# Performance work log

Measured on AMD Instinct MI355X. Metric: run time of the kernel, lower is better.

The kernel has to match this reference:

```python
import jax, jax.numpy as jnp
import numpy as np

HEADS = 16
DIM_HEAD = 64
SCALE = DIM_HEAD ** -0.5


def setup_inputs() -> dict:
    key = jax.random.key(0)
    k1, k2, k3, k4 = jax.random.split(key, 4)
    b, n, dim = 2, 2048, 1024
    inner = HEADS * DIM_HEAD  # 1024
    x = jax.random.normal(k1, (b, n, dim), dtype=jnp.float32)
    mask = jax.random.randint(k2, (b, n), 0, 2, dtype=jnp.int32)
    Wqkv = jax.random.normal(k3, (dim, inner), dtype=jnp.float32) * (dim ** -0.5)
    Wout = jax.random.normal(k4, (inner, dim), dtype=jnp.float32) * (inner ** -0.5)
    bout = jnp.zeros((dim,), dtype=jnp.float32)
    return {"x": x, "mask": mask, "Wqkv": Wqkv, "Wout": Wout, "bout": bout}


def reference(x, mask, Wqkv, Wout, bout):
    b, n, _ = x.shape
    # shared projection: w acts as q = k = v (CRATE subspace attention)
    w = jnp.einsum('bnd,de->bne', x, Wqkv)
    w = w.reshape(b, n, HEADS, DIM_HEAD).transpose(0, 2, 1, 3)  # b h n d
    dots = jnp.einsum('bhid,bhjd->bhij', w, w) * SCALE           # b h n n
    attn = jax.nn.softmax(dots, axis=-1)
    # post-softmax multiplicative masking (mask=1 zeros the column)
    m = mask[:, None, None, :].astype(attn.dtype)
    attn = attn * (1.0 - m)
    out = jnp.einsum('bhij,bhjd->bhid', attn, w)                 # b h n d
    out = out.transpose(0, 2, 1, 3).reshape(b, n, HEADS * DIM_HEAD)
    return jnp.einsum('bne,ed->bnd', out, Wout) + bout
```

## Files before the change

kernel.cpp:

```cpp
#include <hip/hip_runtime.h>
#include <hip/hip_bf16.h>
#include <stdint.h>

typedef unsigned short u16;
typedef unsigned int u32;
typedef __bf16 bf16x8 __attribute__((ext_vector_type(8)));
typedef float f32x4 __attribute__((ext_vector_type(4)));
typedef float f32x16 __attribute__((ext_vector_type(16)));
typedef u32 u32x4 __attribute__((ext_vector_type(4)));

#define AS1 __attribute__((address_space(1)))
#define AS3 __attribute__((address_space(3)))

__device__ __forceinline__ void async16(const u16* g, u16* l) {
  __builtin_amdgcn_global_load_lds((const AS1 uint32_t*)(const void*)g,
                                   (AS3 uint32_t*)l, 16, 0, 0);
}

__device__ __forceinline__ u16 f2bf(float v) {
  union { __hip_bfloat16 b; u16 u; } c; c.b = __float2bfloat16(v); return c.u;
}

__device__ __forceinline__ u32 pkbf(float a, float b) {
  u32 r;
  asm("v_cvt_pk_bf16_f32 %0, %1, %2" : "=v"(r) : "v"(a), "v"(b));
  return r;
}

__device__ __forceinline__ void swap32(u32 &a, u32 &b) {
  asm("v_permlane32_swap_b32 %0, %1" : "+v"(a), "+v"(b));
}

#if __has_builtin(__builtin_amdgcn_exp2f)
#define fast_exp2(x) __builtin_amdgcn_exp2f(x)
#else
#define fast_exp2(x) exp2f(x)
#endif

#if __has_builtin(__builtin_amdgcn_rcpf)
#define fast_rcp(x) __builtin_amdgcn_rcpf(x)
#else
#define fast_rcp(x) (1.0f / (x))
#endif

__device__ __forceinline__ uint4 pack8(float4 lo, float4 hi) {
  uint4 q;
  q.x = (u32)f2bf(lo.x) | ((u32)f2bf(lo.y) << 16);
  q.y = (u32)f2bf(lo.z) | ((u32)f2bf(lo.w) << 16);
  q.z = (u32)f2bf(hi.x) | ((u32)f2bf(hi.y) << 16);
  q.w = (u32)f2bf(hi.z) | ((u32)f2bf(hi.w) << 16);
  return q;
}

__global__ void cvt_x(const float* __restrict__ in, u16* __restrict__ out) {
  int i = (blockIdx.x * 256 + threadIdx.x) * 8;
  float4 lo = *(const float4*)(in + i);
  float4 hi = *(const float4*)(in + i + 4);
  *(uint4*)(out + i) = pack8(lo, hi);
}

__global__ void transpose1024_cvt2(const float* __restrict__ in0, u16* __restrict__ out0,
                                   const float* __restrict__ in1, u16* __restrict__ out1) {
  const float* in = blockIdx.z ? in1 : in0;
  u16* out = blockIdx.z ? out1 : out0;
  __shared__ u16 tile[32][33];
  int tx = threadIdx.x, ty = threadIdx.y;
  int c0 = blockIdx.x * 32, r0 = blockIdx.y * 32;
#pragma unroll
  for (int i = 0; i < 32; i += 8)
    tile[ty + i][tx] = f2bf(in[(size_t)(r0 + ty + i) * 1024 + c0 + tx]);
  __syncthreads();
#pragma unroll
  for (int i = 0; i < 32; i += 8)
    out[(size_t)(c0 + ty + i) * 1024 + r0 + tx] = tile[tx][ty + i];
}

__global__ void scale_transpose_v(const u16* __restrict__ w, const int* __restrict__ mask,
                                  u16* __restrict__ Vt) {
  __shared__ u16 tile[32][33];
  const int tx = threadIdx.x, ty = threadIdx.y;
  const int j0 = blockIdx.x * 32, d0 = blockIdx.y * 32;
  const int bh = blockIdx.z, b = bh >> 4, hc = (bh & 15) * 64;
#pragma unroll
  for (int i = 0; i < 32; i += 8) {
    int j = j0 + ty + i;
    u16 v = w[(size_t)(b * 2048 + j) * 1024 + hc + d0 + tx];
    tile[ty + i][tx] = mask[b * 2048 + j] ? (u16)0 : v;
  }
  __syncthreads();
#pragma unroll
  for (int i = 0; i < 32; i += 8)
    Vt[((size_t)bh * 64 + d0 + ty + i) * 2048 + j0 + tx] = tile[tx][ty + i];
}

template<bool OUT_F32>
__launch_bounds__(256)
__global__ void gemm_bt(const u16* __restrict__ A, const u16* __restrict__ BT,
                        void* __restrict__ Cp, const float* __restrict__ bias,
                        int M, int N, int K) {
  __shared__ __align__(16) u16 As[2][128 * 32];
  __shared__ __align__(16) u16 Bs[2][64 * 32];
  const int t = threadIdx.x;
  const int lane = t & 63, wave = t >> 6;
  const int m0 = blockIdx.x * 128, n0 = blockIdx.y * 64;
  const int wm = (wave & 1) * 64, wn = (wave >> 1) * 32;
  const int lrow = lane & 15, quad = lane >> 4;

  f32x4 acc[4][2] = {};

  const int ar = t >> 2, ac = (t & 3) * 8;
  const u16* gA = A + (size_t)(m0 + ar) * K + ac;
  const u16* gB = BT + (size_t)(n0 + ar) * K + ac;

  for (int k0 = 0; k0 < K; k0 += 64) {
    async16(gA + k0,                       &As[0][t * 8]);
    async16(gA + k0 + (size_t)64 * K,      &As[0][t * 8 + 2048]);
    async16(gA + k0 + 32,                  &As[1][t * 8]);
    async16(gA + k0 + 32 + (size_t)64 * K, &As[1][t * 8 + 2048]);
    async16(gB + k0,                       &Bs[0][t * 8]);
    async16(gB + k0 + 32,                  &Bs[1][t * 8]);
    __syncthreads();

#pragma unroll
    for (int kk = 0; kk < 2; kk++) {
      bf16x8 af[4], bfr[2];
#pragma unroll
      for (int i = 0; i < 4; i++)
        af[i] = *(const bf16x8*)&As[kk][(wm + i * 16 + lrow) * 32 + quad * 8];
#pragma unroll
      for (int j = 0; j < 2; j++)
        bfr[j] = *(const bf16x8*)&Bs[kk][(wn + j * 16 + lrow) * 32 + quad * 8];
#pragma unroll
      for (int i = 0; i < 4; i++)
#pragma unroll
        for (int j = 0; j < 2; j++)
          acc[i][j] = __builtin_amdgcn_mfma_f32_16x16x32_bf16(af[i], bfr[j], acc[i][j], 0, 0, 0);
    }
    __syncthreads();
  }

  float bv[2];
#pragma unroll
  for (int j = 0; j < 2; j++)
    bv[j] = bias ? bias[n0 + wn + j * 16 + lrow] : 0.f;

#pragma unroll
  for (int i = 0; i < 4; i++) {
#pragma unroll
    for (int r = 0; r < 4; r++) {
      int row = m0 + wm + i * 16 + quad * 4 + r;
#pragma unroll
      for (int j = 0; j < 2; j++) {
        size_t ci = (size_t)row * N + n0 + wn + j * 16 + lrow;
        float v = acc[i][j][r] + bv[j];
        if (OUT_F32) ((float*)Cp)[ci] = v;
        else ((u16*)Cp)[ci] = f2bf(v);
      }
    }
  }
}

#define C1 0.18033688f
#define C2 -28.853901f
__launch_bounds__(512)
__global__ void attn_kernel(const u16* __restrict__ w, const u16* __restrict__ Vt,
                            u16* __restrict__ y) {
  __shared__ __align__(16) u16 smem[2][2][2][64 * 64];
  const int t = threadIdx.x, lane = t & 63, wv = t >> 6;
  const int qg = wv & 3, kgr = wv >> 2;
  const int ql = lane & 31, hi = lane >> 5, swz = ql & 7;
  const int bh = blockIdx.y, b = bh >> 4, hc = (bh & 15) * 64;
  const int q0 = blockIdx.x * 128;
  const size_t rowb = (size_t)b * 2048;

  const int tt = t & 255;
  const int sg = t >> 8;
  const int skey = tt >> 3;
  const int scl = ((tt & 7) ^ (skey & 7)) * 8;
  const int sjb = sg * 1024;
  const u16* kptr = w + rowb * 1024 + hc;
  const u16* vptr = Vt + (size_t)bh * 64 * 2048;

  bf16x8 qf[4];
  {
    const size_t qrow = rowb + q0 + qg * 32 + ql;
#pragma unroll
    for (int ks = 0; ks < 4; ks++)
      qf[ks] = *(const bf16x8*)&w[qrow * 1024 + hc + ks * 16 + hi * 8];
  }

  union { u32x4 u; bf16x8 bf; } ones;
  ones.u = (u32x4){0x3F803F80u, 0x3F803F80u, 0x3F803F80u, 0x3F803F80u};

  f32x16 o0 = {}, o1 = {};
  f32x16 den = {};

#define STAGE(buf, j0s) do { \
    async16(kptr + (size_t)(sjb + (j0s) + skey) * 1024 + scl,       &smem[0][sg][buf][tt * 8]); \
    async16(kptr + (size_t)(sjb + (j0s) + skey + 32) * 1024 + scl,  &smem[0][sg][buf][2048 + tt * 8]); \
    async16(vptr + (size_t)skey * 2048 + sjb + (j0s) + scl,         &smem[1][sg][buf][tt * 8]); \
    async16(vptr + (size_t)(skey + 32) * 2048 + sjb + (j0s) + scl,  &smem[1][sg][buf][2048 + tt * 8]); \
  } while (0)

  STAGE(0, 0);
  __syncthreads();

  int cur = 0;
  for (int j0 = 0; j0 < 1024; j0 += 64) {
    if (j0 + 64 < 1024) STAGE(cur ^ 1, j0 + 64);

    const u16* Wt = smem[0][kgr][cur];
    const u16* Vts = smem[1][kgr][cur];

    u32x4 pa[4];
#pragma unroll
    for (int g = 0; g < 2; g++) {
      f32x16 p = {};
#pragma unroll
      for (int ks = 0; ks < 4; ks++) {
        bf16x8 af = *(const bf16x8*)
            &Wt[(g * 32 + ql) * 64 + (((ks * 2 + hi) ^ swz) * 8)];
        p = __builtin_amdgcn_mfma_f32_32x32x16_bf16(af, qf[ks], p, 0, 0, 0);
      }
      float e[16];
#pragma unroll
      for (int r = 0; r < 16; r++)
        e[r] = fast_exp2(fmaf(p[r], C1, C2));
      u32 a0 = pkbf(e[0], e[1]),   b0 = pkbf(e[4], e[5]);   swap32(a0, b0);
      u32 a1 = pkbf(e[2], e[3]),   b1 = pkbf(e[6], e[7]);   swap32(a1, b1);
      u32 a2 = pkbf(e[8], e[9]),   b2 = pkbf(e[12], e[13]); swap32(a2, b2);
      u32 a3 = pkbf(e[10], e[11]), b3 = pkbf(e[14], e[15]); swap32(a3, b3);
      u32x4 f0 = {a0, a1, b0, b1};
      u32x4 f1 = {a2, a3, b2, b3};
      pa[2 * g + 0] = f0;
      pa[2 * g + 1] = f1;
    }

    __builtin_amdgcn_s_setprio(1);
#pragma unroll
    for (int ks = 0; ks < 4; ks++) {
      union { u32x4 u; bf16x8 bf; } cv; cv.u = pa[ks];
      bf16x8 vb0 = *(const bf16x8*)
          &Vts[ql * 64 + (((ks * 2 + hi) ^ swz) * 8)];
      bf16x8 vb1 = *(const bf16x8*)
          &Vts[(32 + ql) * 64 + (((ks * 2 + hi) ^ swz) * 8)];
      o0 = __builtin_amdgcn_mfma_f32_32x32x16_bf16(cv.bf, vb0, o0, 0, 0, 0);
      o1 = __builtin_amdgcn_mfma_f32_32x32x16_bf16(cv.bf, vb1, o1, 0, 0, 0);
      den = __builtin_amdgcn_mfma_f32_32x32x16_bf16(cv.bf, ones.bf, den, 0, 0, 0);
    }
    __builtin_amdgcn_s_setprio(0);

    __syncthreads();
    cur ^= 1;
  }
#undef STAGE

  float* mrg = (float*)smem;
  float* slot = mrg + (qg * 64 + lane) * 49;
  if (kgr == 1) {
#pragma unroll
    for (int r = 0; r < 16; r++) {
      slot[r] = o0[r]; slot[16 + r] = o1[r]; slot[32 + r] = den[r];
    }
  }
  __syncthreads();
  if (kgr == 0) {
#pragma unroll
    for (int r = 0; r < 16; r++) {
      o0[r] += slot[r]; o1[r] += slot[16 + r]; den[r] += slot[32 + r];
    }
#pragma unroll
    for (int r = 0; r < 16; r++) {
      const int qo = (r & 3) + 8 * (r >> 2) + 4 * hi;
      const float iv = fast_rcp(den[r]);
      const size_t orow = rowb + q0 + qg * 32 + qo;
      y[orow * 1024 + hc + ql]      = f2bf(o0[r] * iv);
      y[orow * 1024 + hc + 32 + ql] = f2bf(o1[r] * iv);
    }
  }
}

extern "C" void kernel_launch(void* const* d_in, const int* in_sizes, int n_in,
                              void* d_out, int out_size, void* d_ws, size_t ws_size,
                              hipStream_t stream) {
  const float* x    = (const float*)d_in[0];
  const int* mask   = (const int*)d_in[1];
  const float* Wqkv = (const float*)d_in[2];
  const float* Wout = (const float*)d_in[3];
  const float* bout = (const float*)d_in[4];
  float* out = (float*)d_out;

  u16* w     = (u16*)d_ws;
  u16* y     = w + 4096 * 1024;
  u16* WqkvT = y + 4096 * 1024;
  u16* WoutT = WqkvT + 1024 * 1024;
  u16* Vt    = WoutT + 1024 * 1024;
  u16* xb    = y;

  cvt_x<<<2048, 256, 0, stream>>>(x, xb);
  transpose1024_cvt2<<<dim3(32, 32, 2), dim3(32, 8), 0, stream>>>(Wqkv, WqkvT, Wout, WoutT);
  gemm_bt<false><<<dim3(32, 16), 256, 0, stream>>>(xb, WqkvT, w, nullptr, 4096, 1024, 1024);
  scale_transpose_v<<<dim3(64, 2, 32), dim3(32, 8), 0, stream>>>(w, mask, Vt);
  attn_kernel<<<dim3(16, 32), 512, 0, stream>>>(w, Vt, y);
  gemm_bt<true><<<dim3(32, 16), 256, 0, stream>>>(y, WoutT, out, bout, 4096, 1024, 1024);
}
```

Before: 162.8 us.

## Double-buffer GEMM K-loop and remap workgroups for XCD-aware locality

The GEMM now double-buffers its LDS tiles, prefetching the next K-chunk while the current one feeds the MFMAs, so the load-then-wait barrier no longer serializes every iteration. Both the GEMM and attention kernels remap the linear workgroup ID so that blocks landing on the same XCD (assigned round-robin by ID mod 8) share A/B rows or the same head, which is meant to improve L2 reuse. Doubling the LDS footprint may reduce occupancy. The remapping hardcodes the grid shapes (8x8 chunks in the GEMM, 16 query blocks per head in attention) and would be wrong for other shapes.

```diff
diff --git a/kernel.cpp b/kernel.cpp
--- a/kernel.cpp
+++ b/kernel.cpp
@@ -98,11 +98,14 @@
 __global__ void gemm_bt(const u16* __restrict__ A, const u16* __restrict__ BT,
                         void* __restrict__ Cp, const float* __restrict__ bias,
                         int M, int N, int K) {
-  __shared__ __align__(16) u16 As[2][128 * 32];
-  __shared__ __align__(16) u16 Bs[2][64 * 32];
+  __shared__ __align__(16) u16 As[2][128 * 64];
+  __shared__ __align__(16) u16 Bs[2][64 * 64];
   const int t = threadIdx.x;
   const int lane = t & 63, wave = t >> 6;
-  const int m0 = blockIdx.x * 128, n0 = blockIdx.y * 64;
+  const int wgid = blockIdx.x + gridDim.x * blockIdx.y;
+  const int chunk = wgid & 7, ii = wgid >> 3;
+  const int m0 = ((chunk & 3) * 8 + (ii & 7)) * 128;
+  const int n0 = ((chunk >> 2) * 8 + (ii >> 3)) * 64;
   const int wm = (wave & 1) * 64, wn = (wave >> 1) * 32;
   const int lrow = lane & 15, quad = lane >> 4;
 
@@ -112,24 +115,31 @@
   const u16* gA = A + (size_t)(m0 + ar) * K + ac;
   const u16* gB = BT + (size_t)(n0 + ar) * K + ac;
 
+#define GSTAGE(buf, k0s) do { \
+    async16(gA + (k0s),                       &As[buf][t * 8]); \
+    async16(gA + (k0s) + (size_t)64 * K,      &As[buf][t * 8 + 2048]); \
+    async16(gA + (k0s) + 32,                  &As[buf][4096 + t * 8]); \
+    async16(gA + (k0s) + 32 + (size_t)64 * K, &As[buf][4096 + t * 8 + 2048]); \
+    async16(gB + (k0s),                       &Bs[buf][t * 8]); \
+    async16(gB + (k0s) + 32,                  &Bs[buf][2048 + t * 8]); \
+  } while (0)
+
+  GSTAGE(0, 0);
+  __syncthreads();
+
+  int cur = 0;
   for (int k0 = 0; k0 < K; k0 += 64) {
-    async16(gA + k0,                       &As[0][t * 8]);
-    async16(gA + k0 + (size_t)64 * K,      &As[0][t * 8 + 2048]);
-    async16(gA + k0 + 32,                  &As[1][t * 8]);
-    async16(gA + k0 + 32 + (size_t)64 * K, &As[1][t * 8 + 2048]);
-    async16(gB + k0,                       &Bs[0][t * 8]);
-    async16(gB + k0 + 32,                  &Bs[1][t * 8]);
-    __syncthreads();
+    if (k0 + 64 < K) GSTAGE(cur ^ 1, k0 + 64);
 
 #pragma unroll
     for (int kk = 0; kk < 2; kk++) {
       bf16x8 af[4], bfr[2];
 #pragma unroll
       for (int i = 0; i < 4; i++)
-        af[i] = *(const bf16x8*)&As[kk][(wm + i * 16 + lrow) * 32 + quad * 8];
+        af[i] = *(const bf16x8*)&As[cur][kk * 4096 + (wm + i * 16 + lrow) * 32 + quad * 8];
 #pragma unroll
       for (int j = 0; j < 2; j++)
-        bfr[j] = *(const bf16x8*)&Bs[kk][(wn + j * 16 + lrow) * 32 + quad * 8];
+        bfr[j] = *(const bf16x8*)&Bs[cur][kk * 2048 + (wn + j * 16 + lrow) * 32 + quad * 8];
 #pragma unroll
       for (int i = 0; i < 4; i++)
 #pragma unroll
@@ -137,7 +147,9 @@
           acc[i][j] = __builtin_amdgcn_mfma_f32_16x16x32_bf16(af[i], bfr[j], acc[i][j], 0, 0, 0);
     }
     __syncthreads();
-  }
+    cur ^= 1;
+  }
+#undef GSTAGE
 
   float bv[2];
 #pragma unroll
@@ -169,8 +181,10 @@
   const int t = threadIdx.x, lane = t & 63, wv = t >> 6;
   const int qg = wv & 3, kgr = wv >> 2;
   const int ql = lane & 31, hi = lane >> 5, swz = ql & 7;
-  const int bh = blockIdx.y, b = bh >> 4, hc = (bh & 15) * 64;
-  const int q0 = blockIdx.x * 128;
+  const int wgid = blockIdx.x + 16 * blockIdx.y;
+  const int newid = (wgid & 7) * 64 + (wgid >> 3);
+  const int bh = newid >> 4, b = bh >> 4, hc = (bh & 15) * 64;
+  const int q0 = (newid & 15) * 128;
   const size_t rowb = (size_t)b * 2048;
 
   const int tt = t & 255;
```

Result: no change. 162.2 us (-0.4%).
